# Optimization experiments

Hardware: AMD Instinct MI355X
Metric: run time of the kernel (lower is better)

The kernel has to match this reference:

```python
import jax, jax.numpy as jnp
import numpy as np

NU, NS, DIM, H, DEG, B = 100000, 200000, 64, 2, 8, 16384
HD = H * DIM

def _edges(key, n, deg):
    # random edges plus self-loops (DGL add_self_loop) so every dst has >=1 edge
    src = jax.random.randint(key, (n * deg,), 0, n, dtype=jnp.int32)
    dst = jax.random.randint(jax.random.fold_in(key, 1), (n * deg,), 0, n, dtype=jnp.int32)
    loop = jnp.arange(n, dtype=jnp.int32)
    return jnp.concatenate([src, loop]), jnp.concatenate([dst, loop])

def setup_inputs() -> dict:
    key = jax.random.key(0)
    ks = jax.random.split(key, 24)
    u_src, u_dst = _edges(ks[0], NU, DEG)
    s_src, s_dst = _edges(ks[1], NS, DEG)
    g = lambda k, shp, scale=0.1: jax.random.normal(k, shp, jnp.float32) * scale
    return {
        'userIdx': jax.random.randint(ks[2], (B,), 0, NU, dtype=jnp.int32),
        'servIdx': jax.random.randint(ks[3], (B,), 0, NS, dtype=jnp.int32),
        'u_src': u_src, 'u_dst': u_dst, 's_src': s_src, 's_dst': s_dst,
        'user_emb': g(ks[4], (NU, DIM), 1.0), 'serv_emb': g(ks[5], (NS, DIM), 1.0),
        'u_W': g(ks[6], (DIM, HD)), 'u_attn_l': g(ks[7], (H, DIM)), 'u_attn_r': g(ks[8], (H, DIM)),
        'u_bias': jnp.zeros((HD,), jnp.float32), 'u_ln_g': jnp.ones((HD,), jnp.float32), 'u_ln_b': jnp.zeros((HD,), jnp.float32),
        's_W': g(ks[9], (DIM, HD)), 's_attn_l': g(ks[10], (H, DIM)), 's_attn_r': g(ks[11], (H, DIM)),
        's_bias': jnp.zeros((HD,), jnp.float32), 's_ln_g': jnp.ones((HD,), jnp.float32), 's_ln_b': jnp.zeros((HD,), jnp.float32),
        'W1': g(ks[12], (2 * DIM, 128)), 'b1': jnp.zeros((128,), jnp.float32),
        'ln1_g': jnp.ones((128,), jnp.float32), 'ln1_b': jnp.zeros((128,), jnp.float32),
        'W2': g(ks[13], (128, 128)), 'b2': jnp.zeros((128,), jnp.float32),
        'ln2_g': jnp.ones((128,), jnp.float32), 'ln2_b': jnp.zeros((128,), jnp.float32),
        'W3': g(ks[14], (128, 1)), 'b3': jnp.zeros((1,), jnp.float32),
    }

def _layernorm(x, g, b, eps=1e-5):
    mu = jnp.mean(x, -1, keepdims=True)
    var = jnp.mean(jnp.square(x - mu), -1, keepdims=True)
    return (x - mu) * jax.lax.rsqrt(var + eps) * g + b

def _gat_block(feat, src, dst, W, al, ar, bias, ln_g, ln_b, n):
    # DGL GATConv (eval: dropout = identity), then LayerNorm + ELU + head-mean
    h = (feat @ W).reshape(n, H, DIM)                  # [N,H,D]
    el = jnp.sum(h * al, -1)                           # [N,H]
    er = jnp.sum(h * ar, -1)
    e = jax.nn.leaky_relu(el[src] + er[dst], 0.2)      # [E,H]
    m = jax.ops.segment_max(e, dst, num_segments=n)    # edge softmax per dst
    ex = jnp.exp(e - m[dst])
    den = jax.ops.segment_sum(ex, dst, num_segments=n)
    alpha = ex / den[dst]                              # [E,H]
    out = jax.ops.segment_sum(alpha[:, :, None] * h[src], dst, num_segments=n)
    out = out.reshape(n, HD) + bias                    # [N,H*D]
    out = jax.nn.elu(_layernorm(out, ln_g, ln_b))
    return jnp.mean(out.reshape(n, H, DIM), axis=1)    # [N,D]

def reference(userIdx, servIdx, u_src, u_dst, s_src, s_dst, user_emb, serv_emb,
              u_W, u_attn_l, u_attn_r, u_bias, u_ln_g, u_ln_b,
              s_W, s_attn_l, s_attn_r, s_bias, s_ln_g, s_ln_b,
              W1, b1, ln1_g, ln1_b, W2, b2, ln2_g, ln2_b, W3, b3):
    ug = _gat_block(user_emb, u_src, u_dst, u_W, u_attn_l, u_attn_r, u_bias, u_ln_g, u_ln_b, NU)
    sg = _gat_block(serv_emb, s_src, s_dst, s_W, s_attn_l, s_attn_r, s_bias, s_ln_g, s_ln_b, NS)
    ue = ug[userIdx] + user_emb[userIdx]               # agg == 'add'
    se = sg[servIdx] + serv_emb[servIdx]
    x = jnp.concatenate([ue, se], axis=-1)             # [B, 2*DIM]
    x = jax.nn.relu(_layernorm(x @ W1 + b1, ln1_g, ln1_b))
    x = jax.nn.relu(_layernorm(x @ W2 + b2, ln2_g, ln2_b))
    return jax.nn.sigmoid(x @ W3 + b3).reshape(-1)
```

## Files before the change

kernel.cpp:

```cpp
#include <hip/hip_runtime.h>
#include <cstdint>
#include <cstddef>

__device__ __forceinline__ float rl_f32(float v, int lane) {
    return __uint_as_float((unsigned)__builtin_amdgcn_readlane((int)__float_as_uint(v), lane));
}
__device__ __forceinline__ float wave_sum(float v) {
#pragma unroll
    for (int o = 32; o > 0; o >>= 1) v += __shfl_xor(v, o, 64);
    return v;
}
__device__ __forceinline__ unsigned wave_sum_u32(unsigned v) {
#pragma unroll
    for (int o = 32; o > 0; o >>= 1) v += (unsigned)__shfl_xor((int)v, o, 64);
    return v;
}
__device__ __forceinline__ float wave_max(float v) {
#pragma unroll
    for (int o = 32; o > 0; o >>= 1) v = fmaxf(v, __shfl_xor(v, o, 64));
    return v;
}

__global__ void zero_kernel(unsigned* __restrict__ cnt_u, unsigned char* __restrict__ mark_u, int nU,
                            unsigned* __restrict__ cnt_s, unsigned char* __restrict__ mark_s, int nS) {
    int i = blockIdx.x * blockDim.x + threadIdx.x;
    int tot = nU + nS;
    if (i >= tot) return;
    if (i < nU) { cnt_u[i] = 0u; mark_u[i] = 0; }
    else        { cnt_s[i - nU] = 0u; mark_s[i - nU] = 0; }
}

__global__ void mark_kernel(const int* __restrict__ uIdx, unsigned char* __restrict__ mark_u,
                            const int* __restrict__ sIdx, unsigned char* __restrict__ mark_s, int B) {
    int t = blockIdx.x * blockDim.x + threadIdx.x;
    if (t < B)          mark_u[uIdx[t]] = 1;
    else if (t < 2 * B) mark_s[sIdx[t - B]] = 1;
}

__global__ void count_kernel(const int* __restrict__ u_dst, int EU, unsigned* __restrict__ cnt_u,
                             const unsigned char* __restrict__ mark_u,
                             const int* __restrict__ s_dst, int ES, unsigned* __restrict__ cnt_s,
                             const unsigned char* __restrict__ mark_s) {
    int e = blockIdx.x * blockDim.x + threadIdx.x;
    int tot = EU + ES;
    if (e >= tot) return;
    if (e < EU) {
        int d = u_dst[e];
        if (mark_u[d]) atomicAdd(&cnt_u[d], 1u);
    } else {
        int d = s_dst[e - EU];
        if (mark_s[d]) atomicAdd(&cnt_s[d], 1u);
    }
}

#define SCAN_TPB 256
#define SCAN_VPT 8
#define SCAN_TILE 2048

__global__ __launch_bounds__(SCAN_TPB) void scan1_kernel(
    const unsigned* __restrict__ cnt_u, unsigned* __restrict__ indptr_u, unsigned* __restrict__ sums_u, int nU, int nbU,
    const unsigned* __restrict__ cnt_s, unsigned* __restrict__ indptr_s, unsigned* __restrict__ sums_s, int nS) {
    int b = (int)blockIdx.x;
    const unsigned* cnt; unsigned* indptr; unsigned* sums; int n, tile;
    if (b < nbU) { cnt = cnt_u; indptr = indptr_u; sums = sums_u; n = nU; tile = b; }
    else         { cnt = cnt_s; indptr = indptr_s; sums = sums_s; n = nS; tile = b - nbU; }
    int base = tile * SCAN_TILE + (int)threadIdx.x * SCAN_VPT;
    unsigned v[SCAN_VPT];
#pragma unroll
    for (int j = 0; j < SCAN_VPT; ++j) { int i = base + j; v[j] = (i < n) ? cnt[i] : 0u; }
#pragma unroll
    for (int j = 1; j < SCAN_VPT; ++j) v[j] += v[j - 1];
    __shared__ unsigned sh[SCAN_TPB];
    sh[threadIdx.x] = v[SCAN_VPT - 1];
    __syncthreads();
    for (int d = 1; d < SCAN_TPB; d <<= 1) {
        unsigned t = (threadIdx.x >= (unsigned)d) ? sh[threadIdx.x - d] : 0u;
        __syncthreads();
        sh[threadIdx.x] += t;
        __syncthreads();
    }
    unsigned prefix = (threadIdx.x > 0) ? sh[threadIdx.x - 1] : 0u;
#pragma unroll
    for (int j = 0; j < SCAN_VPT; ++j) { int i = base + j; if (i < n) indptr[i + 1] = v[j] + prefix; }
    if (threadIdx.x == SCAN_TPB - 1) sums[tile] = sh[SCAN_TPB - 1];
}

__global__ __launch_bounds__(SCAN_TPB) void scanf_kernel(
    const unsigned* __restrict__ cnt_u, unsigned* __restrict__ indptr_u, unsigned* __restrict__ fill_u,
    const unsigned* __restrict__ sums_u, int nU, int nbU,
    const unsigned* __restrict__ cnt_s, unsigned* __restrict__ indptr_s, unsigned* __restrict__ fill_s,
    const unsigned* __restrict__ sums_s, int nS) {
    int b = (int)blockIdx.x;
    const unsigned* cnt; unsigned* indptr; unsigned* fill; const unsigned* sums; int n, tile;
    if (b < nbU) { cnt = cnt_u; indptr = indptr_u; fill = fill_u; sums = sums_u; n = nU; tile = b; }
    else         { cnt = cnt_s; indptr = indptr_s; fill = fill_s; sums = sums_s; n = nS; tile = b - nbU; }
    int lane = threadIdx.x & 63;
    unsigned a0 = (lane < tile) ? sums[lane] : 0u;
    unsigned a1 = (lane + 64 < tile) ? sums[lane + 64] : 0u;
    unsigned off = wave_sum_u32(a0 + a1);
    int base = tile * SCAN_TILE + (int)threadIdx.x * SCAN_VPT;
#pragma unroll
    for (int j = 0; j < SCAN_VPT; ++j) {
        int i = base + j;
        if (i < n) {
            unsigned incl = indptr[i + 1] + off;
            indptr[i + 1] = incl;
            fill[i] = incl - cnt[i];
        }
    }
    if (b == 0 && threadIdx.x == 0) { indptr_u[0] = 0u; indptr_s[0] = 0u; }
}

__global__ void scatter_kernel(const int* __restrict__ u_src, const int* __restrict__ u_dst, int EU,
                               unsigned* __restrict__ fill_u, unsigned* __restrict__ csr_u,
                               const unsigned char* __restrict__ mark_u,
                               const int* __restrict__ s_src, const int* __restrict__ s_dst, int ES,
                               unsigned* __restrict__ fill_s, unsigned* __restrict__ csr_s,
                               const unsigned char* __restrict__ mark_s) {
    int e = blockIdx.x * blockDim.x + threadIdx.x;
    int tot = EU + ES;
    if (e >= tot) return;
    if (e < EU) {
        int d = u_dst[e];
        if (mark_u[d]) {
            unsigned pos = atomicAdd(&fill_u[d], 1u);
            csr_u[pos] = (unsigned)u_src[e];
        }
    } else {
        int ee = e - EU;
        int d = s_dst[ee];
        if (mark_s[d]) {
            unsigned pos = atomicAdd(&fill_s[d], 1u);
            csr_s[pos] = (unsigned)s_src[ee];
        }
    }
}

__global__ __launch_bounds__(256) void eler_kernel(
    const float* __restrict__ u_W, const float* __restrict__ u_al, const float* __restrict__ u_ar,
    const float* __restrict__ s_W, const float* __restrict__ s_al, const float* __restrict__ s_ar,
    const float* __restrict__ user_emb, float4* __restrict__ elr_u, int nU,
    const float* __restrict__ serv_emb, float4* __restrict__ elr_s, int nS) {
    __shared__ float4 wq[128];
    int t = threadIdx.x;
    if (t < 128) {
        const float* W  = (t < 64) ? u_W : s_W;
        const float* al = (t < 64) ? u_al : s_al;
        const float* ar = (t < 64) ? u_ar : s_ar;
        int k = t & 63;
        float a0 = 0.f, a1 = 0.f, a2 = 0.f, a3 = 0.f;
        for (int d = 0; d < 64; ++d) {
            float w0 = W[k * 128 + d], w1 = W[k * 128 + 64 + d];
            a0 += w0 * al[d];      a1 += w1 * al[64 + d];
            a2 += w0 * ar[d];      a3 += w1 * ar[64 + d];
        }
        wq[t] = make_float4(a0, a1, a2, a3);
    }
    __syncthreads();
    int n = blockIdx.x * 256 + t;
    int tot = nU + nS;
    if (n >= tot) return;
    const float* feat; const float4* wqp; float4* elr; int i;
    if (n < nU) { i = n;      feat = user_emb + (size_t)i * 64; wqp = wq;      elr = elr_u; }
    else        { i = n - nU; feat = serv_emb + (size_t)i * 64; wqp = wq + 64; elr = elr_s; }
    float a0 = 0.f, a1 = 0.f, a2 = 0.f, a3 = 0.f;
    const float4* f4 = (const float4*)feat;
#pragma unroll
    for (int q = 0; q < 16; ++q) {
        float4 f = f4[q];
        float4 w;
        w = wqp[q * 4 + 0]; a0 = fmaf(f.x, w.x, a0); a1 = fmaf(f.x, w.y, a1); a2 = fmaf(f.x, w.z, a2); a3 = fmaf(f.x, w.w, a3);
        w = wqp[q * 4 + 1]; a0 = fmaf(f.y, w.x, a0); a1 = fmaf(f.y, w.y, a1); a2 = fmaf(f.y, w.z, a2); a3 = fmaf(f.y, w.w, a3);
        w = wqp[q * 4 + 2]; a0 = fmaf(f.z, w.x, a0); a1 = fmaf(f.z, w.y, a1); a2 = fmaf(f.z, w.z, a2); a3 = fmaf(f.z, w.w, a3);
        w = wqp[q * 4 + 3]; a0 = fmaf(f.w, w.x, a0); a1 = fmaf(f.w, w.y, a1); a2 = fmaf(f.w, w.z, a2); a3 = fmaf(f.w, w.w, a3);
    }
    elr[i] = make_float4(a0, a1, a2, a3);
}

__global__ __launch_bounds__(256, 4) void gather_kernel(
    const int* __restrict__ uIdx, const unsigned* __restrict__ indptr_u, const unsigned* __restrict__ csr_u,
    const float* __restrict__ elr_u, const float* __restrict__ user_emb,
    const int* __restrict__ sIdx, const unsigned* __restrict__ indptr_s, const unsigned* __restrict__ csr_s,
    const float* __restrict__ elr_s, const float* __restrict__ serv_emb,
    float* __restrict__ aggbuf, int B, int nBlocksU) {
    bool isU = (int)blockIdx.x < nBlocksU;
    const int* idx; const unsigned* indptr; const unsigned* csr; const float* elr; const float* emb;
    int bb4 = isU ? (int)blockIdx.x : (int)blockIdx.x - nBlocksU;
    if (isU) { idx = uIdx; indptr = indptr_u; csr = csr_u; elr = elr_u; emb = user_emb; }
    else     { idx = sIdx; indptr = indptr_s; csr = csr_s; elr = elr_s; emb = serv_emb; }
    int wid = threadIdx.x >> 6, lane = threadIdx.x & 63;
    int b = bb4 * 4 + wid;
    if (b >= B) return;
    int row = isU ? b : B + b;
    const float2* elr2 = (const float2*)elr;

    int d = idx[b];
    unsigned s = indptr[d];
    int deg = (int)(indptr[d + 1] - s);
    float2 erp = elr2[(size_t)d * 2 + 1];
    float er0 = erp.x, er1 = erp.y;

    float agg0 = 0.f, agg1 = 0.f;
    if (deg <= 64) {
        unsigned mysrc = 0;
        if (lane < deg) mysrc = csr[s + lane];
        float2 elp = elr2[(size_t)mysrc * 2];
        float e0 = elp.x + er0; e0 = e0 > 0.f ? e0 : 0.2f * e0;
        float e1 = elp.y + er1; e1 = e1 > 0.f ? e1 : 0.2f * e1;
        if (lane >= deg) { e0 = -1e30f; e1 = -1e30f; }
        float m0 = wave_max(e0), m1 = wave_max(e1);
        float p0 = (lane < deg) ? expf(e0 - m0) : 0.f;
        float p1 = (lane < deg) ? expf(e1 - m1) : 0.f;
        float sum0 = wave_sum(p0), sum1 = wave_sum(p1);
        float alpha0 = p0 * (1.0f / sum0);
        float alpha1 = p1 * (1.0f / sum1);

        for (int cb = 0; cb < deg; cb += 16) {
            float f[16];
#pragma unroll
            for (int jj = 0; jj < 16; ++jj) {
                int j2 = cb + jj;
                if (j2 < deg) {
                    unsigned sj = (unsigned)__builtin_amdgcn_readlane((int)mysrc, j2);
                    f[jj] = emb[(size_t)sj * 64 + lane];
                } else f[jj] = 0.f;
            }
#pragma unroll
            for (int jj = 0; jj < 16; ++jj) {
                int j2 = cb + jj;
                if (j2 < deg) {
                    agg0 = fmaf(rl_f32(alpha0, j2), f[jj], agg0);
                    agg1 = fmaf(rl_f32(alpha1, j2), f[jj], agg1);
                }
            }
        }
    } else {
        float m0 = -1e30f, m1 = -1e30f;
        for (int j = lane; j < deg; j += 64) {
            int src = (int)csr[s + j];
            float2 elp = elr2[(size_t)src * 2];
            float e0 = elp.x + er0; e0 = e0 > 0.f ? e0 : 0.2f * e0;
            float e1 = elp.y + er1; e1 = e1 > 0.f ? e1 : 0.2f * e1;
            m0 = fmaxf(m0, e0); m1 = fmaxf(m1, e1);
        }
        m0 = wave_max(m0); m1 = wave_max(m1);
        float s0 = 0.f, s1 = 0.f;
        for (int j = lane; j < deg; j += 64) {
            int src = (int)csr[s + j];
            float2 elp = elr2[(size_t)src * 2];
            float e0 = elp.x + er0; e0 = e0 > 0.f ? e0 : 0.2f * e0;
            float e1 = elp.y + er1; e1 = e1 > 0.f ? e1 : 0.2f * e1;
            s0 += expf(e0 - m0); s1 += expf(e1 - m1);
        }
        s0 = wave_sum(s0); s1 = wave_sum(s1);
        float r0 = 1.0f / s0, r1 = 1.0f / s1;
        for (int j = 0; j < deg; ++j) {
            int src = (int)csr[s + j];
            float2 elp = elr2[(size_t)src * 2];
            float e0 = elp.x + er0; e0 = e0 > 0.f ? e0 : 0.2f * e0;
            float e1 = elp.y + er1; e1 = e1 > 0.f ? e1 : 0.2f * e1;
            float a0 = expf(e0 - m0) * r0;
            float a1 = expf(e1 - m1) * r1;
            float f = emb[(size_t)src * 64 + lane];
            agg0 = fmaf(a0, f, agg0); agg1 = fmaf(a1, f, agg1);
        }
    }

    aggbuf[(size_t)row * 128 + lane] = agg0;
    aggbuf[(size_t)row * 128 + 64 + lane] = agg1;
}

#define PROJ_RPW 16
__global__ __launch_bounds__(256) void proj_kernel(
    const int* __restrict__ uIdx, const float* __restrict__ u_W, const float* __restrict__ u_bias,
    const float* __restrict__ u_g, const float* __restrict__ u_b, const float* __restrict__ user_emb,
    const int* __restrict__ sIdx, const float* __restrict__ s_W, const float* __restrict__ s_bias,
    const float* __restrict__ s_g, const float* __restrict__ s_b, const float* __restrict__ serv_emb,
    const float* __restrict__ aggbuf, float* __restrict__ xbuf, int B, int nBlocksU) {
    __shared__ float2 Wp[64 * 64];
    bool isU = (int)blockIdx.x < nBlocksU;
    const int* idx; const float* W; const float* bias; const float* g; const float* bb; const float* emb;
    int bbase;
    if (isU) { idx = uIdx; W = u_W; bias = u_bias; g = u_g; bb = u_b; emb = user_emb; bbase = (int)blockIdx.x; }
    else     { idx = sIdx; W = s_W; bias = s_bias; g = s_g; bb = s_b; emb = serv_emb; bbase = (int)blockIdx.x - nBlocksU; }
    for (int t = threadIdx.x; t < 4096; t += 256) {
        int k = t >> 6, l = t & 63;
        Wp[t] = make_float2(W[k * 128 + l], W[k * 128 + 64 + l]);
    }
    __syncthreads();

    int wid = threadIdx.x >> 6, lane = threadIdx.x & 63;
    int xoff = isU ? 0 : 64;
    int rowoff = isU ? 0 : B;
    float biasa = bias[lane], biasb = bias[64 + lane];
    float ga = g[lane], gb2 = g[64 + lane];
    float ba = bb[lane], bb2 = bb[64 + lane];

    int gwave = bbase * 4 + wid;
    int rstart = gwave * PROJ_RPW;
    for (int r0 = rstart; r0 < rstart + PROJ_RPW && r0 < B; r0 += 4) {
        float agg0[4], agg1[4], embv[4];
#pragma unroll
        for (int j = 0; j < 4; ++j) {
            int b = r0 + j;
            if (b < B) {
                int d = idx[b];
                embv[j] = emb[(size_t)d * 64 + lane];
                agg0[j] = aggbuf[(size_t)(rowoff + b) * 128 + lane];
                agg1[j] = aggbuf[(size_t)(rowoff + b) * 128 + 64 + lane];
            } else { embv[j] = 0.f; agg0[j] = 0.f; agg1[j] = 0.f; }
        }
        float acc0[4] = {0.f, 0.f, 0.f, 0.f}, acc1[4] = {0.f, 0.f, 0.f, 0.f};
#pragma unroll
        for (int k = 0; k < 64; ++k) {
            float2 w = Wp[k * 64 + lane];
#pragma unroll
            for (int j = 0; j < 4; ++j) {
                acc0[j] = fmaf(rl_f32(agg0[j], k), w.x, acc0[j]);
                acc1[j] = fmaf(rl_f32(agg1[j], k), w.y, acc1[j]);
            }
        }
#pragma unroll
        for (int j = 0; j < 4; ++j) {
            int b = r0 + j;
            if (b >= B) break;
            float o0 = acc0[j] + biasa, o1 = acc1[j] + biasb;
            float tot = wave_sum(o0 + o1);
            float mu = tot * (1.0f / 128.0f);
            float d0 = o0 - mu, d1 = o1 - mu;
            float var = wave_sum(d0 * d0 + d1 * d1) * (1.0f / 128.0f);
            float rstd = rsqrtf(var + 1e-5f);
            float l0 = d0 * rstd * ga + ba;
            float l1 = d1 * rstd * gb2 + bb2;
            l0 = l0 > 0.f ? l0 : expm1f(l0);
            l1 = l1 > 0.f ? l1 : expm1f(l1);
            float v = 0.5f * (l0 + l1) + embv[j];
            xbuf[(size_t)b * 128 + xoff + lane] = v;
        }
    }
}

#define MLP_RPW 8
__global__ __launch_bounds__(256) void mlp_kernel(const float* __restrict__ xin, float* __restrict__ xout,
                                                  const float* __restrict__ W, const float* __restrict__ bvec,
                                                  const float* __restrict__ g, const float* __restrict__ bb,
                                                  int B) {
    __shared__ float2 Wp[128 * 64];
    for (int t = threadIdx.x; t < 8192; t += 256) {
        int k = t >> 6, l = t & 63;
        Wp[t] = make_float2(W[k * 128 + l], W[k * 128 + 64 + l]);
    }
    __syncthreads();
    int wid = threadIdx.x >> 6, lane = threadIdx.x & 63;
    int gwave = (int)blockIdx.x * 4 + wid;
    int rstart = gwave * MLP_RPW;
    for (int r0 = rstart; r0 < rstart + MLP_RPW && r0 < B; r0 += 4) {
        float x0[4], x1[4];
#pragma unroll
        for (int j = 0; j < 4; ++j) {
            int r = r0 + j;
            if (r < B) {
                x0[j] = xin[(size_t)r * 128 + lane];
                x1[j] = xin[(size_t)r * 128 + 64 + lane];
            } else { x0[j] = 0.f; x1[j] = 0.f; }
        }
        float acc0[4] = {0.f, 0.f, 0.f, 0.f}, acc1[4] = {0.f, 0.f, 0.f, 0.f};
#pragma unroll
        for (int k = 0; k < 64; ++k) {
            float2 w = Wp[k * 64 + lane];
#pragma unroll
            for (int j = 0; j < 4; ++j) {
                float xv = rl_f32(x0[j], k);
                acc0[j] = fmaf(xv, w.x, acc0[j]); acc1[j] = fmaf(xv, w.y, acc1[j]);
            }
        }
#pragma unroll
        for (int k = 0; k < 64; ++k) {
            float2 w = Wp[(64 + k) * 64 + lane];
#pragma unroll
            for (int j = 0; j < 4; ++j) {
                float xv = rl_f32(x1[j], k);
                acc0[j] = fmaf(xv, w.x, acc0[j]); acc1[j] = fmaf(xv, w.y, acc1[j]);
            }
        }
#pragma unroll
        for (int j = 0; j < 4; ++j) {
            int r = r0 + j;
            if (r >= B) break;
            float o0 = acc0[j] + bvec[lane], o1 = acc1[j] + bvec[64 + lane];
            float tot = wave_sum(o0 + o1);
            float mu = tot * (1.0f / 128.0f);
            float d0 = o0 - mu, d1 = o1 - mu;
            float var = wave_sum(d0 * d0 + d1 * d1) * (1.0f / 128.0f);
            float rstd = rsqrtf(var + 1e-5f);
            float l0 = d0 * rstd * g[lane] + bb[lane];
            float l1 = d1 * rstd * g[64 + lane] + bb[64 + lane];
            l0 = fmaxf(l0, 0.f); l1 = fmaxf(l1, 0.f);
            xout[(size_t)r * 128 + lane] = l0;
            xout[(size_t)r * 128 + 64 + lane] = l1;
        }
    }
}

__global__ __launch_bounds__(256) void mlpfin_kernel(const float* __restrict__ xin, float* __restrict__ out,
                                                     const float* __restrict__ W, const float* __restrict__ bvec,
                                                     const float* __restrict__ g, const float* __restrict__ bb,
                                                     const float* __restrict__ W3, const float* __restrict__ b3,
                                                     int B) {
    __shared__ float2 Wp[128 * 64];
    for (int t = threadIdx.x; t < 8192; t += 256) {
        int k = t >> 6, l = t & 63;
        Wp[t] = make_float2(W[k * 128 + l], W[k * 128 + 64 + l]);
    }
    __syncthreads();
    int wid = threadIdx.x >> 6, lane = threadIdx.x & 63;
    float w3a = W3[lane], w3b = W3[64 + lane];
    float b3v = b3[0];
    int gwave = (int)blockIdx.x * 4 + wid;
    int rstart = gwave * MLP_RPW;
    for (int r0 = rstart; r0 < rstart + MLP_RPW && r0 < B; r0 += 4) {
        float x0[4], x1[4];
#pragma unroll
        for (int j = 0; j < 4; ++j) {
            int r = r0 + j;
            if (r < B) {
                x0[j] = xin[(size_t)r * 128 + lane];
                x1[j] = xin[(size_t)r * 128 + 64 + lane];
            } else { x0[j] = 0.f; x1[j] = 0.f; }
        }
        float acc0[4] = {0.f, 0.f, 0.f, 0.f}, acc1[4] = {0.f, 0.f, 0.f, 0.f};
#pragma unroll
        for (int k = 0; k < 64; ++k) {
            float2 w = Wp[k * 64 + lane];
#pragma unroll
            for (int j = 0; j < 4; ++j) {
                float xv = rl_f32(x0[j], k);
                acc0[j] = fmaf(xv, w.x, acc0[j]); acc1[j] = fmaf(xv, w.y, acc1[j]);
            }
        }
#pragma unroll
        for (int k = 0; k < 64; ++k) {
            float2 w = Wp[(64 + k) * 64 + lane];
#pragma unroll
            for (int j = 0; j < 4; ++j) {
                float xv = rl_f32(x1[j], k);
                acc0[j] = fmaf(xv, w.x, acc0[j]); acc1[j] = fmaf(xv, w.y, acc1[j]);
            }
        }
#pragma unroll
        for (int j = 0; j < 4; ++j) {
            int r = r0 + j;
            if (r >= B) break;
            float o0 = acc0[j] + bvec[lane], o1 = acc1[j] + bvec[64 + lane];
            float tot = wave_sum(o0 + o1);
            float mu = tot * (1.0f / 128.0f);
            float d0 = o0 - mu, d1 = o1 - mu;
            float var = wave_sum(d0 * d0 + d1 * d1) * (1.0f / 128.0f);
            float rstd = rsqrtf(var + 1e-5f);
            float l0 = d0 * rstd * g[lane] + bb[lane];
            float l1 = d1 * rstd * g[64 + lane] + bb[64 + lane];
            l0 = fmaxf(l0, 0.f); l1 = fmaxf(l1, 0.f);
            float acc = wave_sum(fmaf(l0, w3a, l1 * w3b)) + b3v;
            if (lane == 0) out[r] = 1.0f / (1.0f + expf(-acc));
        }
    }
}

extern "C" void kernel_launch(void* const* d_in, const int* in_sizes, int n_in,
                              void* d_out, int out_size, void* d_ws, size_t ws_size,
                              hipStream_t stream) {
    const int*   userIdx  = (const int*)d_in[0];
    const int*   servIdx  = (const int*)d_in[1];
    const int*   u_src    = (const int*)d_in[2];
    const int*   u_dst    = (const int*)d_in[3];
    const int*   s_src    = (const int*)d_in[4];
    const int*   s_dst    = (const int*)d_in[5];
    const float* user_emb = (const float*)d_in[6];
    const float* serv_emb = (const float*)d_in[7];
    const float* u_W      = (const float*)d_in[8];
    const float* u_al     = (const float*)d_in[9];
    const float* u_ar     = (const float*)d_in[10];
    const float* u_bias   = (const float*)d_in[11];
    const float* u_ln_g   = (const float*)d_in[12];
    const float* u_ln_b   = (const float*)d_in[13];
    const float* s_W      = (const float*)d_in[14];
    const float* s_al     = (const float*)d_in[15];
    const float* s_ar     = (const float*)d_in[16];
    const float* s_bias   = (const float*)d_in[17];
    const float* s_ln_g   = (const float*)d_in[18];
    const float* s_ln_b   = (const float*)d_in[19];
    const float* W1       = (const float*)d_in[20];
    const float* b1       = (const float*)d_in[21];
    const float* ln1_g    = (const float*)d_in[22];
    const float* ln1_b    = (const float*)d_in[23];
    const float* W2       = (const float*)d_in[24];
    const float* b2       = (const float*)d_in[25];
    const float* ln2_g    = (const float*)d_in[26];
    const float* ln2_b    = (const float*)d_in[27];
    const float* W3       = (const float*)d_in[28];
    const float* b3       = (const float*)d_in[29];

    const int B  = in_sizes[0];
    const int EU = in_sizes[2];
    const int ES = in_sizes[4];
    const int NU = in_sizes[6] / 64;
    const int NS = in_sizes[7] / 64;

    char* w = (char*)d_ws;
    size_t off = 0;
    auto alloc = [&](size_t bytes) -> void* {
        void* p = w + off;
        off = (off + bytes + 255) & ~(size_t)255;
        return p;
    };
    unsigned* cnt_u    = (unsigned*)alloc((size_t)NU * 4);
    unsigned char* mark_u = (unsigned char*)alloc((size_t)NU);
    unsigned* indptr_u = (unsigned*)alloc((size_t)(NU + 1) * 4);
    unsigned* fill_u   = (unsigned*)alloc((size_t)NU * 4);
    unsigned* csr_u    = (unsigned*)alloc((size_t)EU * 4);
    unsigned* cnt_s    = (unsigned*)alloc((size_t)NS * 4);
    unsigned char* mark_s = (unsigned char*)alloc((size_t)NS);
    unsigned* indptr_s = (unsigned*)alloc((size_t)(NS + 1) * 4);
    unsigned* fill_s   = (unsigned*)alloc((size_t)NS * 4);
    unsigned* csr_s    = (unsigned*)alloc((size_t)ES * 4);
    unsigned* sums_u   = (unsigned*)alloc(256 * 4);
    unsigned* sums_s   = (unsigned*)alloc(256 * 4);
    float*    elr_u    = (float*)   alloc((size_t)NU * 4 * sizeof(float));
    float*    elr_s    = (float*)   alloc((size_t)NS * 4 * sizeof(float));
    float*    aggbuf   = (float*)   alloc((size_t)2 * B * 128 * sizeof(float));
    float*    xbuf     = (float*)   alloc((size_t)B * 128 * sizeof(float));
    float*    ybuf     = aggbuf;
    (void)ws_size;

    const int nbU = (NU + SCAN_TILE - 1) / SCAN_TILE;
    const int nbS = (NS + SCAN_TILE - 1) / SCAN_TILE;
    const int totN = NU + NS;
    const int totE = EU + ES;

    zero_kernel<<<(totN + 255) / 256, 256, 0, stream>>>(cnt_u, mark_u, NU, cnt_s, mark_s, NS);
    mark_kernel<<<(2 * B + 255) / 256, 256, 0, stream>>>(userIdx, mark_u, servIdx, mark_s, B);
    count_kernel<<<(totE + 255) / 256, 256, 0, stream>>>(u_dst, EU, cnt_u, mark_u,
                                                         s_dst, ES, cnt_s, mark_s);
    scan1_kernel<<<nbU + nbS, SCAN_TPB, 0, stream>>>(cnt_u, indptr_u, sums_u, NU, nbU,
                                                     cnt_s, indptr_s, sums_s, NS);
    scanf_kernel<<<nbU + nbS, SCAN_TPB, 0, stream>>>(cnt_u, indptr_u, fill_u, sums_u, NU, nbU,
                                                     cnt_s, indptr_s, fill_s, sums_s, NS);
    scatter_kernel<<<(totE + 255) / 256, 256, 0, stream>>>(u_src, u_dst, EU, fill_u, csr_u, mark_u,
                                                           s_src, s_dst, ES, fill_s, csr_s, mark_s);
    eler_kernel<<<(totN + 255) / 256, 256, 0, stream>>>(u_W, u_al, u_ar, s_W, s_al, s_ar,
                                                        user_emb, (float4*)elr_u, NU,
                                                        serv_emb, (float4*)elr_s, NS);
    const int nBlocksU = (B + 3) / 4;
    gather_kernel<<<2 * nBlocksU, 256, 0, stream>>>(
        userIdx, indptr_u, csr_u, elr_u, user_emb,
        servIdx, indptr_s, csr_s, elr_s, serv_emb,
        aggbuf, B, nBlocksU);
    const int nPB = (B + 4 * PROJ_RPW - 1) / (4 * PROJ_RPW);
    proj_kernel<<<2 * nPB, 256, 0, stream>>>(
        userIdx, u_W, u_bias, u_ln_g, u_ln_b, user_emb,
        servIdx, s_W, s_bias, s_ln_g, s_ln_b, serv_emb,
        aggbuf, xbuf, B, nPB);
    const int nMB = (B + 4 * MLP_RPW - 1) / (4 * MLP_RPW);
    mlp_kernel<<<nMB, 256, 0, stream>>>(xbuf, ybuf, W1, b1, ln1_g, ln1_b, B);
    mlpfin_kernel<<<nMB, 256, 0, stream>>>(ybuf, (float*)d_out, W2, b2, ln2_g, ln2_b, W3, b3, B);
}
```

Baseline: 419.2 us.

## Stage activation tiles in LDS and stream weights from global in projection/MLP kernels

The projection and two MLP kernels now stage a 16-row activation tile in shared memory and read weights directly from global (cache-resident) memory. Each block handles 16 rows, 4 per wave, instead of first copying the full weight matrix into LDS and broadcasting activations with readlane. This drops the per-block weight staging cost and the scalar readlane chain. In exchange there are more blocks, repeated global weight loads per block, and an unguarded tile load that assumes B is a multiple of 16.

After: 388.7 us. 7.3% less time.

```diff
diff --git a/kernel.cpp b/kernel.cpp
--- a/kernel.cpp
+++ b/kernel.cpp
@@ -2,23 +2,23 @@
 #include <cstdint>
 #include <cstddef>
 
+__device__ __forceinline__ float wave_sum(float v) {
+#pragma unroll
+    for (int o = 32; o > 0; o >>= 1) v += __shfl_xor(v, o, 64);
+    return v;
+}
+__device__ __forceinline__ unsigned wave_sum_u32(unsigned v) {
+#pragma unroll
+    for (int o = 32; o > 0; o >>= 1) v += (unsigned)__shfl_xor((int)v, o, 64);
+    return v;
+}
+__device__ __forceinline__ float wave_max(float v) {
+#pragma unroll
+    for (int o = 32; o > 0; o >>= 1) v = fmaxf(v, __shfl_xor(v, o, 64));
+    return v;
+}
 __device__ __forceinline__ float rl_f32(float v, int lane) {
     return __uint_as_float((unsigned)__builtin_amdgcn_readlane((int)__float_as_uint(v), lane));
-}
-__device__ __forceinline__ float wave_sum(float v) {
-#pragma unroll
-    for (int o = 32; o > 0; o >>= 1) v += __shfl_xor(v, o, 64);
-    return v;
-}
-__device__ __forceinline__ unsigned wave_sum_u32(unsigned v) {
-#pragma unroll
-    for (int o = 32; o > 0; o >>= 1) v += (unsigned)__shfl_xor((int)v, o, 64);
-    return v;
-}
-__device__ __forceinline__ float wave_max(float v) {
-#pragma unroll
-    for (int o = 32; o > 0; o >>= 1) v = fmaxf(v, __shfl_xor(v, o, 64));
-    return v;
 }
 
 __global__ void zero_kernel(unsigned* __restrict__ cnt_u, unsigned char* __restrict__ mark_u, int nU,
@@ -270,135 +270,134 @@
     aggbuf[(size_t)row * 128 + 64 + lane] = agg1;
 }
 
-#define PROJ_RPW 16
+#define PROJ_ROWS 16
 __global__ __launch_bounds__(256) void proj_kernel(
     const int* __restrict__ uIdx, const float* __restrict__ u_W, const float* __restrict__ u_bias,
     const float* __restrict__ u_g, const float* __restrict__ u_b, const float* __restrict__ user_emb,
     const int* __restrict__ sIdx, const float* __restrict__ s_W, const float* __restrict__ s_bias,
     const float* __restrict__ s_g, const float* __restrict__ s_b, const float* __restrict__ serv_emb,
-    const float* __restrict__ aggbuf, float* __restrict__ xbuf, int B, int nBlocksU) {
-    __shared__ float2 Wp[64 * 64];
-    bool isU = (int)blockIdx.x < nBlocksU;
+    const float* __restrict__ aggbuf, float* __restrict__ xbuf, int B, int nPB) {
+    __shared__ __align__(16) float xs[PROJ_ROWS][128];
+    bool isU = (int)blockIdx.x < nPB;
     const int* idx; const float* W; const float* bias; const float* g; const float* bb; const float* emb;
-    int bbase;
-    if (isU) { idx = uIdx; W = u_W; bias = u_bias; g = u_g; bb = u_b; emb = user_emb; bbase = (int)blockIdx.x; }
-    else     { idx = sIdx; W = s_W; bias = s_bias; g = s_g; bb = s_b; emb = serv_emb; bbase = (int)blockIdx.x - nBlocksU; }
-    for (int t = threadIdx.x; t < 4096; t += 256) {
-        int k = t >> 6, l = t & 63;
-        Wp[t] = make_float2(W[k * 128 + l], W[k * 128 + 64 + l]);
-    }
-    __syncthreads();
+    int blk = isU ? (int)blockIdx.x : (int)blockIdx.x - nPB;
+    if (isU) { idx = uIdx; W = u_W; bias = u_bias; g = u_g; bb = u_b; emb = user_emb; }
+    else     { idx = sIdx; W = s_W; bias = s_bias; g = s_g; bb = s_b; emb = serv_emb; }
+    int r0 = blk * PROJ_ROWS;
+    int rowoff = isU ? 0 : B;
+
+    {
+        const float4* src4 = (const float4*)(aggbuf + (size_t)(rowoff + r0) * 128);
+        float4* xs4 = (float4*)xs;
+#pragma unroll
+        for (int i = 0; i < 2; ++i) xs4[threadIdx.x + i * 256] = src4[threadIdx.x + i * 256];
+    }
 
     int wid = threadIdx.x >> 6, lane = threadIdx.x & 63;
     int xoff = isU ? 0 : 64;
-    int rowoff = isU ? 0 : B;
+
+    float embv[4]; int rb[4];
+#pragma unroll
+    for (int j = 0; j < 4; ++j) {
+        rb[j] = r0 + wid * 4 + j;
+        int d = (rb[j] < B) ? idx[rb[j]] : 0;
+        embv[j] = emb[(size_t)d * 64 + lane];
+    }
+    __syncthreads();
+
+    float acc0[4] = {0.f, 0.f, 0.f, 0.f}, acc1[4] = {0.f, 0.f, 0.f, 0.f};
+    for (int kq = 0; kq < 16; ++kq) {
+        float w0[4], w1[4];
+#pragma unroll
+        for (int i = 0; i < 4; ++i) {
+            w0[i] = W[(kq * 4 + i) * 128 + lane];
+            w1[i] = W[(kq * 4 + i) * 128 + 64 + lane];
+        }
+#pragma unroll
+        for (int j = 0; j < 4; ++j) {
+            int r = wid * 4 + j;
+            float4 xa = *(const float4*)&xs[r][kq * 4];
+            float4 xb = *(const float4*)&xs[r][64 + kq * 4];
+            acc0[j] = fmaf(xa.x, w0[0], acc0[j]); acc0[j] = fmaf(xa.y, w0[1], acc0[j]);
+            acc0[j] = fmaf(xa.z, w0[2], acc0[j]); acc0[j] = fmaf(xa.w, w0[3], acc0[j]);
+            acc1[j] = fmaf(xb.x, w1[0], acc1[j]); acc1[j] = fmaf(xb.y, w1[1], acc1[j]);
+            acc1[j] = fmaf(xb.z, w1[2], acc1[j]); acc1[j] = fmaf(xb.w, w1[3], acc1[j]);
+        }
+    }
+
     float biasa = bias[lane], biasb = bias[64 + lane];
     float ga = g[lane], gb2 = g[64 + lane];
     float ba = bb[lane], bb2 = bb[64 + lane];
-
-    int gwave = bbase * 4 + wid;
-    int rstart = gwave * PROJ_RPW;
-    for (int r0 = rstart; r0 < rstart + PROJ_RPW && r0 < B; r0 += 4) {
-        float agg0[4], agg1[4], embv[4];
-#pragma unroll
-        for (int j = 0; j < 4; ++j) {
-            int b = r0 + j;
-            if (b < B) {
-                int d = idx[b];
-                embv[j] = emb[(size_t)d * 64 + lane];
-                agg0[j] = aggbuf[(size_t)(rowoff + b) * 128 + lane];
-                agg1[j] = aggbuf[(size_t)(rowoff + b) * 128 + 64 + lane];
-            } else { embv[j] = 0.f; agg0[j] = 0.f; agg1[j] = 0.f; }
-        }
-        float acc0[4] = {0.f, 0.f, 0.f, 0.f}, acc1[4] = {0.f, 0.f, 0.f, 0.f};
-#pragma unroll
-        for (int k = 0; k < 64; ++k) {
-            float2 w = Wp[k * 64 + lane];
-#pragma unroll
-            for (int j = 0; j < 4; ++j) {
-                acc0[j] = fmaf(rl_f32(agg0[j], k), w.x, acc0[j]);
-                acc1[j] = fmaf(rl_f32(agg1[j], k), w.y, acc1[j]);
-            }
-        }
-#pragma unroll
-        for (int j = 0; j < 4; ++j) {
-            int b = r0 + j;
-            if (b >= B) break;
-            float o0 = acc0[j] + biasa, o1 = acc1[j] + biasb;
-            float tot = wave_sum(o0 + o1);
-            float mu = tot * (1.0f / 128.0f);
-            float d0 = o0 - mu, d1 = o1 - mu;
-            float var = wave_sum(d0 * d0 + d1 * d1) * (1.0f / 128.0f);
-            float rstd = rsqrtf(var + 1e-5f);
-            float l0 = d0 * rstd * ga + ba;
-            float l1 = d1 * rstd * gb2 + bb2;
-            l0 = l0 > 0.f ? l0 : expm1f(l0);
-            l1 = l1 > 0.f ? l1 : expm1f(l1);
-            float v = 0.5f * (l0 + l1) + embv[j];
-            xbuf[(size_t)b * 128 + xoff + lane] = v;
-        }
-    }
-}
-
-#define MLP_RPW 8
+#pragma unroll
+    for (int j = 0; j < 4; ++j) {
+        if (rb[j] >= B) break;
+        float o0 = acc0[j] + biasa, o1 = acc1[j] + biasb;
+        float tot = wave_sum(o0 + o1);
+        float mu = tot * (1.0f / 128.0f);
+        float d0 = o0 - mu, d1 = o1 - mu;
+        float var = wave_sum(d0 * d0 + d1 * d1) * (1.0f / 128.0f);
+        float rstd = rsqrtf(var + 1e-5f);
+        float l0 = d0 * rstd * ga + ba;
+        float l1 = d1 * rstd * gb2 + bb2;
+        l0 = l0 > 0.f ? l0 : expm1f(l0);
+        l1 = l1 > 0.f ? l1 : expm1f(l1);
+        xbuf[(size_t)rb[j] * 128 + xoff + lane] = 0.5f * (l0 + l1) + embv[j];
+    }
+}
+
+#define MLP_ROWS 16
 __global__ __launch_bounds__(256) void mlp_kernel(const float* __restrict__ xin, float* __restrict__ xout,
                                                   const float* __restrict__ W, const float* __restrict__ bvec,
                                                   const float* __restrict__ g, const float* __restrict__ bb,
                                                   int B) {
-    __shared__ float2 Wp[128 * 64];
-    for (int t = threadIdx.x; t < 8192; t += 256) {
-        int k = t >> 6, l = t & 63;
-        Wp[t] = make_float2(W[k * 128 + l], W[k * 128 + 64 + l]);
+    __shared__ __align__(16) float xs[MLP_ROWS][128];
+    int r0 = (int)blockIdx.x * MLP_ROWS;
+    {
+        const float4* src4 = (const float4*)(xin + (size_t)r0 * 128);
+        float4* xs4 = (float4*)xs;
+#pragma unroll
+        for (int i = 0; i < 2; ++i) xs4[threadIdx.x + i * 256] = src4[threadIdx.x + i * 256];
     }
     __syncthreads();
     int wid = threadIdx.x >> 6, lane = threadIdx.x & 63;
-    int gwave = (int)blockIdx.x * 4 + wid;
-    int rstart = gwave * MLP_RPW;
-    for (int r0 = rstart; r0 < rstart + MLP_RPW && r0 < B; r0 += 4) {
-        float x0[4], x1[4];
+
+    float acc0[4] = {0.f, 0.f, 0.f, 0.f}, acc1[4] = {0.f, 0.f, 0.f, 0.f};
+    for (int kq = 0; kq < 32; ++kq) {
+        float w0[4], w1[4];
+#pragma unroll
+        for (int i = 0; i < 4; ++i) {
+            w0[i] = W[(kq * 4 + i) * 128 + lane];
+            w1[i] = W[(kq * 4 + i) * 128 + 64 + lane];
+        }
 #pragma unroll
         for (int j = 0; j < 4; ++j) {
-            int r = r0 + j;
-            if (r < B) {
-                x0[j] = xin[(size_t)r * 128 + lane];
-                x1[j] = xin[(size_t)r * 128 + 64 + lane];
-            } else { x0[j] = 0.f; x1[j] = 0.f; }
-        }
-        float acc0[4] = {0.f, 0.f, 0.f, 0.f}, acc1[4] = {0.f, 0.f, 0.f, 0.f};
-#pragma unroll
-        for (int k = 0; k < 64; ++k) {
-            float2 w = Wp[k * 64 + lane];
-#pragma unroll
-            for (int j = 0; j < 4; ++j) {
-                float xv = rl_f32(x0[j], k);
-                acc0[j] = fmaf(xv, w.x, acc0[j]); acc1[j] = fmaf(xv, w.y, acc1[j]);
-            }
-        }
-#pragma unroll
-        for (int k = 0; k < 64; ++k) {
-            float2 w = Wp[(64 + k) * 64 + lane];
-#pragma unroll
-            for (int j = 0; j < 4; ++j) {
-                float xv = rl_f32(x1[j], k);
-                acc0[j] = fmaf(xv, w.x, acc0[j]); acc1[j] = fmaf(xv, w.y, acc1[j]);
-            }
-        }
-#pragma unroll
-        for (int j = 0; j < 4; ++j) {
-            int r = r0 + j;
-            if (r >= B) break;
-            float o0 = acc0[j] + bvec[lane], o1 = acc1[j] + bvec[64 + lane];
-            float tot = wave_sum(o0 + o1);
-            float mu = tot * (1.0f / 128.0f);
-            float d0 = o0 - mu, d1 = o1 - mu;
-            float var = wave_sum(d0 * d0 + d1 * d1) * (1.0f / 128.0f);
-            float rstd = rsqrtf(var + 1e-5f);
-            float l0 = d0 * rstd * g[lane] + bb[lane];
-            float l1 = d1 * rstd * g[64 + lane] + bb[64 + lane];
-            l0 = fmaxf(l0, 0.f); l1 = fmaxf(l1, 0.f);
-            xout[(size_t)r * 128 + lane] = l0;
-            xout[(size_t)r * 128 + 64 + lane] = l1;
-        }
+            int r = wid * 4 + j;
+            float4 xq = *(const float4*)&xs[r][kq * 4];
+            acc0[j] = fmaf(xq.x, w0[0], acc0[j]); acc1[j] = fmaf(xq.x, w1[0], acc1[j]);
+            acc0[j] = fmaf(xq.y, w0[1], acc0[j]); acc1[j] = fmaf(xq.y, w1[1], acc1[j]);
+            acc0[j] = fmaf(xq.z, w0[2], acc0[j]); acc1[j] = fmaf(xq.z, w1[2], acc1[j]);
+            acc0[j] = fmaf(xq.w, w0[3], acc0[j]); acc1[j] = fmaf(xq.w, w1[3], acc1[j]);
+        }
+    }
+
+    float bva = bvec[lane], bvb = bvec[64 + lane];
+    float ga = g[lane], gb2 = g[64 + lane];
+    float ba = bb[lane], bb2 = bb[64 + lane];
+#pragma unroll
+    for (int j = 0; j < 4; ++j) {
+        int r = r0 + wid * 4 + j;
+        if (r >= B) break;
+        float o0 = acc0[j] + bva, o1 = acc1[j] + bvb;
+        float tot = wave_sum(o0 + o1);
+        float mu = tot * (1.0f / 128.0f);
+        float d0 = o0 - mu, d1 = o1 - mu;
+        float var = wave_sum(d0 * d0 + d1 * d1) * (1.0f / 128.0f);
+        float rstd = rsqrtf(var + 1e-5f);
+        float l0 = d0 * rstd * ga + ba;
+        float l1 = d1 * rstd * gb2 + bb2;
+        l0 = fmaxf(l0, 0.f); l1 = fmaxf(l1, 0.f);
+        xout[(size_t)r * 128 + lane] = l0;
+        xout[(size_t)r * 128 + 64 + lane] = l1;
     }
 }
 
@@ -407,62 +406,56 @@
                                                      const float* __restrict__ g, const float* __restrict__ bb,
                                                      const float* __restrict__ W3, const float* __restrict__ b3,
                                                      int B) {
-    __shared__ float2 Wp[128 * 64];
-    for (int t = threadIdx.x; t < 8192; t += 256) {
-        int k = t >> 6, l = t & 63;
-        Wp[t] = make_float2(W[k * 128 + l], W[k * 128 + 64 + l]);
+    __shared__ __align__(16) float xs[MLP_ROWS][128];
+    int r0 = (int)blockIdx.x * MLP_ROWS;
+    {
+        const float4* src4 = (const float4*)(xin + (size_t)r0 * 128);
+        float4* xs4 = (float4*)xs;
+#pragma unroll
+        for (int i = 0; i < 2; ++i) xs4[threadIdx.x + i * 256] = src4[threadIdx.x + i * 256];
     }
     __syncthreads();
     int wid = threadIdx.x >> 6, lane = threadIdx.x & 63;
+
+    float acc0[4] = {0.f, 0.f, 0.f, 0.f}, acc1[4] = {0.f, 0.f, 0.f, 0.f};
+    for (int kq = 0; kq < 32; ++kq) {
+        float w0[4], w1[4];
+#pragma unroll
+        for (int i = 0; i < 4; ++i) {
+            w0[i] = W[(kq * 4 + i) * 128 + lane];
+            w1[i] = W[(kq * 4 + i) * 128 + 64 + lane];
+        }
+#pragma unroll
+        for (int j = 0; j < 4; ++j) {
+            int r = wid * 4 + j;
+            float4 xq = *(const float4*)&xs[r][kq * 4];
+            acc0[j] = fmaf(xq.x, w0[0], acc0[j]); acc1[j] = fmaf(xq.x, w1[0], acc1[j]);
+            acc0[j] = fmaf(xq.y, w0[1], acc0[j]); acc1[j] = fmaf(xq.y, w1[1], acc1[j]);
+            acc0[j] = fmaf(xq.z, w0[2], acc0[j]); acc1[j] = fmaf(xq.z, w1[2], acc1[j]);
+            acc0[j] = fmaf(xq.w, w0[3], acc0[j]); acc1[j] = fmaf(xq.w, w1[3], acc1[j]);
+        }
+    }
+
+    float bva = bvec[lane], bvb = bvec[64 + lane];
+    float ga = g[lane], gb2 = g[64 + lane];
+    float ba = bb[lane], bb2 = bb[64 + lane];
     float w3a = W3[lane], w3b = W3[64 + lane];
     float b3v = b3[0];
-    int gwave = (int)blockIdx.x * 4 + wid;
-    int rstart = gwave * MLP_RPW;
-    for (int r0 = rstart; r0 < rstart + MLP_RPW && r0 < B; r0 += 4) {
-        float x0[4], x1[4];
-#pragma unroll
-        for (int j = 0; j < 4; ++j) {
-            int r = r0 + j;
-            if (r < B) {
-                x0[j] = xin[(size_t)r * 128 + lane];
-                x1[j] = xin[(size_t)r * 128 + 64 + lane];
-            } else { x0[j] = 0.f; x1[j] = 0.f; }
-        }
-        float acc0[4] = {0.f, 0.f, 0.f, 0.f}, acc1[4] = {0.f, 0.f, 0.f, 0.f};
-#pragma unroll
-        for (int k = 0; k < 64; ++k) {
-            float2 w = Wp[k * 64 + lane];
-#pragma unroll
-            for (int j = 0; j < 4; ++j) {
-                float xv = rl_f32(x0[j], k);
-                acc0[j] = fmaf(xv, w.x, acc0[j]); acc1[j] = fmaf(xv, w.y, acc1[j]);
-            }
-        }
-#pragma unroll
-        for (int k = 0; k < 64; ++k) {
-            float2 w = Wp[(64 + k) * 64 + lane];
-#pragma unroll
-            for (int j = 0; j < 4; ++j) {
-                float xv = rl_f32(x1[j], k);
-                acc0[j] = fmaf(xv, w.x, acc0[j]); acc1[j] = fmaf(xv, w.y, acc1[j]);
-            }
-        }
-#pragma unroll
-        for (int j = 0; j < 4; ++j) {
-            int r = r0 + j;
-            if (r >= B) break;
-            float o0 = acc0[j] + bvec[lane], o1 = acc1[j] + bvec[64 + lane];
-            float tot = wave_sum(o0 + o1);
-            float mu = tot * (1.0f / 128.0f);
-            float d0 = o0 - mu, d1 = o1 - mu;
-            float var = wave_sum(d0 * d0 + d1 * d1) * (1.0f / 128.0f);
-            float rstd = rsqrtf(var + 1e-5f);
-            float l0 = d0 * rstd * g[lane] + bb[lane];
-            float l1 = d1 * rstd * g[64 + lane] + bb[64 + lane];
-            l0 = fmaxf(l0, 0.f); l1 = fmaxf(l1, 0.f);
-            float acc = wave_sum(fmaf(l0, w3a, l1 * w3b)) + b3v;
-            if (lane == 0) out[r] = 1.0f / (1.0f + expf(-acc));
-        }
+#pragma unroll
+    for (int j = 0; j < 4; ++j) {
+        int r = r0 + wid * 4 + j;
+        if (r >= B) break;
+        float o0 = acc0[j] + bva, o1 = acc1[j] + bvb;
+        float tot = wave_sum(o0 + o1);
+        float mu = tot * (1.0f / 128.0f);
+        float d0 = o0 - mu, d1 = o1 - mu;
+        float var = wave_sum(d0 * d0 + d1 * d1) * (1.0f / 128.0f);
+        float rstd = rsqrtf(var + 1e-5f);
+        float l0 = d0 * rstd * ga + ba;
+        float l1 = d1 * rstd * gb2 + bb2;
+        l0 = fmaxf(l0, 0.f); l1 = fmaxf(l1, 0.f);
+        float acc = wave_sum(fmaf(l0, w3a, l1 * w3b)) + b3v;
+        if (lane == 0) out[r] = 1.0f / (1.0f + expf(-acc));
     }
 }
 
@@ -555,12 +548,12 @@
         userIdx, indptr_u, csr_u, elr_u, user_emb,
         servIdx, indptr_s, csr_s, elr_s, serv_emb,
         aggbuf, B, nBlocksU);
-    const int nPB = (B + 4 * PROJ_RPW - 1) / (4 * PROJ_RPW);
+    const int nPB = (B + PROJ_ROWS - 1) / PROJ_ROWS;
     proj_kernel<<<2 * nPB, 256, 0, stream>>>(
         userIdx, u_W, u_bias, u_ln_g, u_ln_b, user_emb,
         servIdx, s_W, s_bias, s_ln_g, s_ln_b, serv_emb,
         aggbuf, xbuf, B, nPB);
-    const int nMB = (B + 4 * MLP_RPW - 1) / (4 * MLP_RPW);
+    const int nMB = (B + MLP_ROWS - 1) / MLP_ROWS;
     mlp_kernel<<<nMB, 256, 0, stream>>>(xbuf, ybuf, W1, b1, ln1_g, ln1_b, B);
     mlpfin_kernel<<<nMB, 256, 0, stream>>>(ybuf, (float*)d_out, W2, b2, ln2_g, ln2_b, W3, b3, B);
 }
```
